# Optimization experiments

Measured on AMD Instinct MI355X. Metric: run time of the kernel, lower is better.

## Reference

```python
import jax, jax.numpy as jnp
import numpy as np

B, S, H, E, TOP_K = 4, 4096, 4096, 64, 2

def setup_inputs() -> dict:
    key = jax.random.key(0)
    k1, k2 = jax.random.split(key)
    hidden_states = jax.random.normal(k1, (B, S, H), dtype=jnp.float32)
    gate_weight = jax.random.normal(k2, (E, H), dtype=jnp.float32) * (H ** -0.5)
    return {"hidden_states": hidden_states, "gate_weight": gate_weight}

def reference(hidden_states, gate_weight):
    # gate: logits[b,s,e] = hidden[b,s,h] @ W[e,h]^T (nn.Linear, no bias)
    router_logits = jnp.einsum('bsh,eh->bse', hidden_states, gate_weight)
    router_probs = jax.nn.softmax(router_logits, axis=-1)
    # top-k over experts, then renormalize the selected weights
    expert_weights, expert_indices = jax.lax.top_k(router_probs, TOP_K)
    expert_weights = expert_weights / jnp.sum(expert_weights, axis=-1, keepdims=True)
    return (router_probs, expert_indices, expert_weights)
```

## Files before the change

kernel.cpp:

```cpp
#include <hip/hip_runtime.h>
#include <math.h>

#define TOKENS 16384
#define HDIM 4096
#define NE 64

#define BM 64
#define BK 64
#define NT (HDIM / BK)
#define LP 68
#define TSZ (BM * BK)

typedef float f32x4 __attribute__((ext_vector_type(4)));
typedef int i32x4 __attribute__((ext_vector_type(4)));
typedef __bf16 bf16x8 __attribute__((ext_vector_type(8)));

__device__ __forceinline__ void split8(f32x4 v0, f32x4 v1, i32x4& h, i32x4& l) {
  float x[8];
#pragma unroll
  for (int j = 0; j < 4; ++j) { x[j] = v0[j]; x[4 + j] = v1[j]; }
  union { unsigned short u[8]; i32x4 v; } H, L;
#pragma unroll
  for (int j = 0; j < 8; ++j) {
    __bf16 hb = (__bf16)x[j];
    H.u[j] = __builtin_bit_cast(unsigned short, hb);
    L.u[j] = __builtin_bit_cast(unsigned short, (__bf16)(x[j] - (float)hb));
  }
  h = H.v; l = L.v;
}

__device__ __forceinline__ f32x4 mfma_bf16(i32x4 a, i32x4 b, f32x4 c) {
  return __builtin_amdgcn_mfma_f32_16x16x32_bf16(
      __builtin_bit_cast(bf16x8, a), __builtin_bit_cast(bf16x8, b), c, 0, 0, 0);
}

__global__ __launch_bounds__(256) void convert_w(const float* __restrict__ W,
                                                 unsigned short* __restrict__ Wh,
                                                 unsigned short* __restrict__ Wl) {
  const int i = (blockIdx.x * 256 + threadIdx.x) * 8;
  f32x4 v0 = *(const f32x4*)(W + i);
  f32x4 v1 = *(const f32x4*)(W + i + 4);
  i32x4 h, l;
  split8(v0, v1, h, l);
  *(i32x4*)(Wh + i) = h;
  *(i32x4*)(Wl + i) = l;
}

__global__ __launch_bounds__(512, 2) void router_mfma(const float* __restrict__ A,
                                                      const unsigned short* __restrict__ Wh,
                                                      const unsigned short* __restrict__ Wl,
                                                      float* __restrict__ out) {
  __shared__ __align__(16) unsigned short smem[2 * 4 * TSZ];
  unsigned short* buf0 = smem;
  unsigned short* buf1 = smem + 4 * TSZ;

  const int tid = threadIdx.x;
  const int bt = blockIdx.x;

  const int srow = tid >> 3;
  const int sc = tid & 7;
  const int soff = srow * BK + ((sc ^ (srow & 7)) << 3);

  const float* Ab = A + (size_t)(bt * BM + srow) * HDIM + sc * 8;
  const unsigned short* Whb = Wh + srow * HDIM + sc * 8;
  const unsigned short* Wlb = Wl + srow * HDIM + sc * 8;

  const int lane = tid & 63;
  const int wv = tid >> 6;
  const int tg = wv & 3;
  const int eg = wv >> 2;
  const int l15 = lane & 15;
  const int l7 = lane & 7;
  const int fko = lane >> 4;
  const int arow = tg * 16 + l15;
  const int brow = eg * 32 + l15;

  f32x4 acc0 = {0.f, 0.f, 0.f, 0.f};
  f32x4 acc1 = {0.f, 0.f, 0.f, 0.f};

  f32x4 a0_0, a1_0, a0_1, a1_1;
  i32x4 wh_0, wl_0, wh_1, wl_1;

  auto loadS = [&](int t, f32x4& a0, f32x4& a1, i32x4& wh, i32x4& wl) {
    const int kc = t * BK;
    a0 = *(const f32x4*)(Ab + kc);
    a1 = *(const f32x4*)(Ab + kc + 4);
    wh = *(const i32x4*)(Whb + kc);
    wl = *(const i32x4*)(Wlb + kc);
  };

  auto stage = [&](unsigned short* B, f32x4 a0, f32x4 a1, i32x4 wh, i32x4 wl) {
    i32x4 h, l;
    split8(a0, a1, h, l);
    *(i32x4*)&B[soff] = h;
    *(i32x4*)&B[TSZ + soff] = l;
    *(i32x4*)&B[2 * TSZ + soff] = wh;
    *(i32x4*)&B[3 * TSZ + soff] = wl;
  };

  auto compute = [&](const unsigned short* B) {
    const unsigned short* AhS = B;
    const unsigned short* AlS = B + TSZ;
    const unsigned short* WhS = B + 2 * TSZ;
    const unsigned short* WlS = B + 3 * TSZ;
#pragma unroll
    for (int ks = 0; ks < 2; ++ks) {
      const int ch = ks * 4 + fko;
      const int aoff = arow * BK + ((ch ^ l7) << 3);
      const int boff = brow * BK + ((ch ^ l7) << 3);
      i32x4 fah = *(const i32x4*)&AhS[aoff];
      i32x4 fal = *(const i32x4*)&AlS[aoff];
      i32x4 fbh0 = *(const i32x4*)&WhS[boff];
      i32x4 fbh1 = *(const i32x4*)&WhS[boff + 16 * BK];
      i32x4 fbl0 = *(const i32x4*)&WlS[boff];
      i32x4 fbl1 = *(const i32x4*)&WlS[boff + 16 * BK];
      acc0 = mfma_bf16(fah, fbh0, acc0);
      acc1 = mfma_bf16(fah, fbh1, acc1);
      acc0 = mfma_bf16(fal, fbh0, acc0);
      acc1 = mfma_bf16(fal, fbh1, acc1);
      acc0 = mfma_bf16(fah, fbl0, acc0);
      acc1 = mfma_bf16(fah, fbl1, acc1);
    }
  };

  loadS(0, a0_0, a1_0, wh_0, wl_0);
  stage(buf0, a0_0, a1_0, wh_0, wl_0);
  loadS(1, a0_1, a1_1, wh_1, wl_1);
  __syncthreads();

  for (int t = 0; t < NT; t += 2) {
    compute(buf0);
    if (t + 2 < NT) loadS(t + 2, a0_0, a1_0, wh_0, wl_0);
    stage(buf1, a0_1, a1_1, wh_1, wl_1);
    __syncthreads();

    compute(buf1);
    if (t + 3 < NT) loadS(t + 3, a0_1, a1_1, wh_1, wl_1);
    if (t + 2 < NT) stage(buf0, a0_0, a1_0, wh_0, wl_0);
    __syncthreads();
  }

  float* L = (float*)smem;
#pragma unroll
  for (int r = 0; r < 4; ++r) {
    const int row = tg * 16 + fko * 4 + r;
    L[row * LP + eg * 32 + l15] = acc0[r];
    L[row * LP + eg * 32 + 16 + l15] = acc1[r];
  }
  __syncthreads();

  const int wv8 = tid >> 6;
#pragma unroll
  for (int r = 0; r < 8; ++r) {
    const int lt = wv8 * 8 + r;
    const int tok = bt * BM + lt;
    const float l = L[lt * LP + lane];

    float m = l;
#pragma unroll
    for (int off = 32; off >= 1; off >>= 1) m = fmaxf(m, __shfl_xor(m, off, 64));

    const float e = expf(l - m);
    float sum = e;
#pragma unroll
    for (int off = 32; off >= 1; off >>= 1) sum += __shfl_xor(sum, off, 64);

    const float p = e / sum;
    out[(size_t)tok * NE + lane] = p;

    float m0 = p;
#pragma unroll
    for (int off = 32; off >= 1; off >>= 1) m0 = fmaxf(m0, __shfl_xor(m0, off, 64));
    const unsigned long long b0 = __ballot(p == m0);
    const int i0 = __ffsll(b0) - 1;

    const float pm = (lane == i0) ? -1.f : p;
    float m1 = pm;
#pragma unroll
    for (int off = 32; off >= 1; off >>= 1) m1 = fmaxf(m1, __shfl_xor(m1, off, 64));
    const unsigned long long b1 = __ballot(pm == m1);
    const int i1 = __ffsll(b1) - 1;

    if (lane == 0) {
      float* idxo = out + (size_t)TOKENS * NE + (size_t)tok * 2;
      idxo[0] = (float)i0;
      idxo[1] = (float)i1;
      float* wo = out + (size_t)TOKENS * NE + (size_t)TOKENS * 2 + (size_t)tok * 2;
      const float d = m0 + m1;
      wo[0] = m0 / d;
      wo[1] = m1 / d;
    }
  }
}

extern "C" void kernel_launch(void* const* d_in, const int* in_sizes, int n_in,
                              void* d_out, int out_size, void* d_ws, size_t ws_size,
                              hipStream_t stream) {
  const float* A = (const float*)d_in[0];
  const float* W = (const float*)d_in[1];
  float* out = (float*)d_out;
  unsigned short* Whi = (unsigned short*)d_ws;
  unsigned short* Wlo = Whi + (size_t)NE * HDIM;

  convert_w<<<dim3(NE * HDIM / (256 * 8)), 256, 0, stream>>>(W, Whi, Wlo);
  router_mfma<<<dim3(TOKENS / BM), 512, 0, stream>>>(A, Whi, Wlo, out);
}
```

Before: 394.2 us.

## Split-K router GEMM into partial sums with separate softmax/top-k finalize kernel

Splits the hidden dimension into four K-slices so the grid has four times as many blocks. Each block uses 256 threads with every wave covering all 64 experts, and writes fp32 partial logits to workspace. A new finalize kernel sums the partials and does the softmax and top-2 selection. This targets low occupancy and latency from having only 256 blocks. The cost is extra global traffic for the partial logits, a third kernel launch, and a padded unswizzled LDS layout with a smaller BK.

```diff
diff --git a/kernel.cpp b/kernel.cpp
--- a/kernel.cpp
+++ b/kernel.cpp
@@ -6,10 +6,12 @@
 #define NE 64
 
 #define BM 64
-#define BK 64
-#define NT (HDIM / BK)
-#define LP 68
-#define TSZ (BM * BK)
+#define BK 32
+#define KSPLIT 4
+#define KSLICE (HDIM / KSPLIT)
+#define NT (KSLICE / BK)
+#define WPAD 40
+#define TSZ (64 * WPAD)
 
 typedef float f32x4 __attribute__((ext_vector_type(4)));
 typedef int i32x4 __attribute__((ext_vector_type(4)));
@@ -46,37 +48,36 @@
   *(i32x4*)(Wl + i) = l;
 }
 
-__global__ __launch_bounds__(512, 2) void router_mfma(const float* __restrict__ A,
+__global__ __launch_bounds__(256, 4) void router_gemm(const float* __restrict__ A,
                                                       const unsigned short* __restrict__ Wh,
                                                       const unsigned short* __restrict__ Wl,
-                                                      float* __restrict__ out) {
+                                                      float* __restrict__ P) {
   __shared__ __align__(16) unsigned short smem[2 * 4 * TSZ];
   unsigned short* buf0 = smem;
   unsigned short* buf1 = smem + 4 * TSZ;
 
   const int tid = threadIdx.x;
   const int bt = blockIdx.x;
-
-  const int srow = tid >> 3;
-  const int sc = tid & 7;
-  const int soff = srow * BK + ((sc ^ (srow & 7)) << 3);
-
-  const float* Ab = A + (size_t)(bt * BM + srow) * HDIM + sc * 8;
-  const unsigned short* Whb = Wh + srow * HDIM + sc * 8;
-  const unsigned short* Wlb = Wl + srow * HDIM + sc * 8;
+  const int ks = blockIdx.y;
+
+  const int srow = tid >> 2;
+  const int sc = tid & 3;
+  const int soff = srow * WPAD + sc * 8;
+
+  const float* Ab = A + (size_t)(bt * BM + srow) * HDIM + ks * KSLICE + sc * 8;
+  const unsigned short* Whb = Wh + (size_t)srow * HDIM + ks * KSLICE + sc * 8;
+  const unsigned short* Wlb = Wl + (size_t)srow * HDIM + ks * KSLICE + sc * 8;
 
   const int lane = tid & 63;
-  const int wv = tid >> 6;
-  const int tg = wv & 3;
-  const int eg = wv >> 2;
+  const int tg = tid >> 6;
   const int l15 = lane & 15;
-  const int l7 = lane & 7;
   const int fko = lane >> 4;
-  const int arow = tg * 16 + l15;
-  const int brow = eg * 32 + l15;
-
-  f32x4 acc0 = {0.f, 0.f, 0.f, 0.f};
-  f32x4 acc1 = {0.f, 0.f, 0.f, 0.f};
+  const int aoff = (tg * 16 + l15) * WPAD + fko * 8;
+  const int boff0 = l15 * WPAD + fko * 8;
+
+  f32x4 acc[4];
+#pragma unroll
+  for (int e = 0; e < 4; ++e) acc[e] = (f32x4){0.f, 0.f, 0.f, 0.f};
 
   f32x4 a0_0, a1_0, a0_1, a1_1;
   i32x4 wh_0, wl_0, wh_1, wl_1;
@@ -103,23 +104,15 @@
     const unsigned short* AlS = B + TSZ;
     const unsigned short* WhS = B + 2 * TSZ;
     const unsigned short* WlS = B + 3 * TSZ;
-#pragma unroll
-    for (int ks = 0; ks < 2; ++ks) {
-      const int ch = ks * 4 + fko;
-      const int aoff = arow * BK + ((ch ^ l7) << 3);
-      const int boff = brow * BK + ((ch ^ l7) << 3);
-      i32x4 fah = *(const i32x4*)&AhS[aoff];
-      i32x4 fal = *(const i32x4*)&AlS[aoff];
-      i32x4 fbh0 = *(const i32x4*)&WhS[boff];
-      i32x4 fbh1 = *(const i32x4*)&WhS[boff + 16 * BK];
-      i32x4 fbl0 = *(const i32x4*)&WlS[boff];
-      i32x4 fbl1 = *(const i32x4*)&WlS[boff + 16 * BK];
-      acc0 = mfma_bf16(fah, fbh0, acc0);
-      acc1 = mfma_bf16(fah, fbh1, acc1);
-      acc0 = mfma_bf16(fal, fbh0, acc0);
-      acc1 = mfma_bf16(fal, fbh1, acc1);
-      acc0 = mfma_bf16(fah, fbl0, acc0);
-      acc1 = mfma_bf16(fah, fbl1, acc1);
+    i32x4 ah = *(const i32x4*)&AhS[aoff];
+    i32x4 al = *(const i32x4*)&AlS[aoff];
+#pragma unroll
+    for (int e = 0; e < 4; ++e) {
+      i32x4 wh = *(const i32x4*)&WhS[boff0 + e * 16 * WPAD];
+      i32x4 wl = *(const i32x4*)&WlS[boff0 + e * 16 * WPAD];
+      acc[e] = mfma_bf16(ah, wh, acc[e]);
+      acc[e] = mfma_bf16(al, wh, acc[e]);
+      acc[e] = mfma_bf16(ah, wl, acc[e]);
     }
   };
 
@@ -140,56 +133,58 @@
     __syncthreads();
   }
 
-  float* L = (float*)smem;
-#pragma unroll
-  for (int r = 0; r < 4; ++r) {
-    const int row = tg * 16 + fko * 4 + r;
-    L[row * LP + eg * 32 + l15] = acc0[r];
-    L[row * LP + eg * 32 + 16 + l15] = acc1[r];
-  }
-  __syncthreads();
-
-  const int wv8 = tid >> 6;
-#pragma unroll
-  for (int r = 0; r < 8; ++r) {
-    const int lt = wv8 * 8 + r;
-    const int tok = bt * BM + lt;
-    const float l = L[lt * LP + lane];
-
-    float m = l;
-#pragma unroll
-    for (int off = 32; off >= 1; off >>= 1) m = fmaxf(m, __shfl_xor(m, off, 64));
-
-    const float e = expf(l - m);
-    float sum = e;
-#pragma unroll
-    for (int off = 32; off >= 1; off >>= 1) sum += __shfl_xor(sum, off, 64);
-
-    const float p = e / sum;
-    out[(size_t)tok * NE + lane] = p;
-
-    float m0 = p;
-#pragma unroll
-    for (int off = 32; off >= 1; off >>= 1) m0 = fmaxf(m0, __shfl_xor(m0, off, 64));
-    const unsigned long long b0 = __ballot(p == m0);
-    const int i0 = __ffsll(b0) - 1;
-
-    const float pm = (lane == i0) ? -1.f : p;
-    float m1 = pm;
-#pragma unroll
-    for (int off = 32; off >= 1; off >>= 1) m1 = fmaxf(m1, __shfl_xor(m1, off, 64));
-    const unsigned long long b1 = __ballot(pm == m1);
-    const int i1 = __ffsll(b1) - 1;
-
-    if (lane == 0) {
-      float* idxo = out + (size_t)TOKENS * NE + (size_t)tok * 2;
-      idxo[0] = (float)i0;
-      idxo[1] = (float)i1;
-      float* wo = out + (size_t)TOKENS * NE + (size_t)TOKENS * 2 + (size_t)tok * 2;
-      const float d = m0 + m1;
-      wo[0] = m0 / d;
-      wo[1] = m1 / d;
-    }
+  float* Pb = P + ((size_t)ks * TOKENS + (size_t)bt * BM) * NE;
+#pragma unroll
+  for (int e = 0; e < 4; ++e)
+#pragma unroll
+    for (int r = 0; r < 4; ++r)
+      Pb[(size_t)(tg * 16 + fko * 4 + r) * NE + e * 16 + l15] = acc[e][r];
+}
+
+__global__ __launch_bounds__(256) void router_finalize(const float* __restrict__ P,
+                                                       float* __restrict__ out) {
+  const int lane = threadIdx.x & 63;
+  const int wave = threadIdx.x >> 6;
+  const int tok = blockIdx.x * 4 + wave;
+
+  float l = 0.f;
+#pragma unroll
+  for (int s = 0; s < KSPLIT; ++s)
+    l += P[((size_t)s * TOKENS + tok) * NE + lane];
+
+  float m = l;
+#pragma unroll
+  for (int off = 32; off >= 1; off >>= 1) m = fmaxf(m, __shfl_xor(m, off, 64));
+
+  const float e = expf(l - m);
+  float sum = e;
+#pragma unroll
+  for (int off = 32; off >= 1; off >>= 1) sum += __shfl_xor(sum, off, 64);
+
+  const float p = e / sum;
+  out[(size_t)tok * NE + lane] = p;
+
+  float m0 = p;
+#pragma unroll
+  for (int off = 32; off >= 1; off >>= 1) m0 = fmaxf(m0, __shfl_xor(m0, off, 64));
+  const unsigned long long b0 = __ballot(p == m0);
+  const int i0 = __ffsll(b0) - 1;
+
+  const float pm = (lane == i0) ? -1.f : p;
+  float m1 = pm;
+#pragma unroll
+  for (int off = 32; off >= 1; off >>= 1) m1 = fmaxf(m1, __shfl_xor(m1, off, 64));
+  const unsigned long long b1 = __ballot(pm == m1);
+  const int i1 = __ffsll(b1) - 1;
+
+  if (lane == 0) {
+    float* idxo = out + (size_t)TOKENS * NE + (size_t)tok * 2;
+    idxo[0] = (float)i0;
+    idxo[1] = (float)i1;
+    float* wo = out + (size_t)TOKENS * NE + (size_t)TOKENS * 2 + (size_t)tok * 2;
+    const float d = m0 + m1;
+    wo[0] = m0 / d;
+    wo[1] = m1 / d;
   }
 }
 
@@ -201,7 +196,9 @@
   float* out = (float*)d_out;
   unsigned short* Whi = (unsigned short*)d_ws;
   unsigned short* Wlo = Whi + (size_t)NE * HDIM;
+  float* P = (float*)(Wlo + (size_t)NE * HDIM);
 
   convert_w<<<dim3(NE * HDIM / (256 * 8)), 256, 0, stream>>>(W, Whi, Wlo);
-  router_mfma<<<dim3(TOKENS / BM), 512, 0, stream>>>(A, Whi, Wlo, out);
-}
+  router_gemm<<<dim3(TOKENS / BM, KSPLIT), 256, 0, stream>>>(A, Whi, Wlo, P);
+  router_finalize<<<dim3(TOKENS / 4), 256, 0, stream>>>(P, out);
+}
```

Measured after the change: 396.1 us. Within noise of the previous version (+0.5%).
